# Optimization experiments

Hardware: AMD Instinct MI355X
Metric: run time of the kernel (lower is better)

The kernel has to match this reference:

```python
import jax, jax.numpy as jnp
import numpy as np

VOC, OUT, HID, CUR = 50257, 512, 64, 16
B, S = 32, 4096
EPS = 1e-5


def _ln(x, g, b):
    m = jnp.mean(x, axis=-1, keepdims=True)
    v = jnp.mean((x - m) ** 2, axis=-1, keepdims=True)
    return (x - m) * jax.lax.rsqrt(v + EPS) * g + b


def setup_inputs() -> dict:
    key = jax.random.key(0)
    ks = jax.random.split(key, 12)
    sd = 0.02
    return {
        "x": jax.random.randint(ks[0], (B, S), 0, VOC, dtype=jnp.int64),
        "emb": jax.random.normal(ks[1], (VOC, CUR), jnp.float32) * sd,
        "Wq": jax.random.normal(ks[2], (CUR, CUR), jnp.float32) * sd,
        "bq": jnp.zeros((CUR,), jnp.float32),
        "Wk": jax.random.normal(ks[3], (CUR, CUR), jnp.float32) * sd,
        "bk": jnp.zeros((CUR,), jnp.float32),
        "Wv": jax.random.normal(ks[4], (CUR, CUR), jnp.float32) * sd,
        "bv": jnp.zeros((CUR,), jnp.float32),
        "g_lim": jnp.ones((CUR,), jnp.float32),
        "b_lim": jnp.zeros((CUR,), jnp.float32),
        "Ws": jax.random.normal(ks[5], (HID + CUR, HID), jnp.float32) * sd,
        "bs": jnp.zeros((HID,), jnp.float32),
        "g_doubt": jnp.ones((HID,), jnp.float32),
        "b_doubt": jnp.zeros((HID,), jnp.float32),
        "Wd": jax.random.normal(ks[6], (HID + CUR, OUT), jnp.float32) * sd,
        "bd": jnp.zeros((OUT,), jnp.float32),
        "g_check": jnp.ones((OUT,), jnp.float32),
        "b_check": jnp.zeros((OUT,), jnp.float32),
    }


def reference(x, emb, Wq, bq, Wk, bk, Wv, bv, g_lim, b_lim, Ws, bs,
              g_doubt, b_doubt, Wd, bd, g_check, b_check):
    Bsz, Slen = x.shape
    n_chunks = Slen // CUR
    # [n_chunks, B, CUR] token ids per chunk
    xc = x.reshape(Bsz, n_chunks, CUR).transpose(1, 0, 2)
    sus0 = jnp.zeros((Bsz, CUR, HID), emb.dtype)
    scale = 1.0 / np.sqrt(CUR)

    def step(sus, ids):
        read = emb[ids]                                  # [B, CUR, CUR]
        q = read @ Wq + bq
        k = read @ Wk + bk
        v = read @ Wv + bv
        scores = jnp.einsum('bqd,bkd->bqk', q, k) * scale
        watch = jnp.einsum('bqk,bkd->bqd', jax.nn.softmax(scores, axis=-1), v)
        watch = _ln(watch, g_lim, b_lim)                 # dropout = identity (eval)
        combined = jnp.concatenate([watch, sus], axis=-1)  # [B, CUR, HID+CUR]
        sus_new = _ln(jax.nn.gelu(combined @ Ws + bs, approximate=False),
                      g_doubt, b_doubt)
        out = _ln(combined @ Wd + bd, g_check, b_check)  # [B, CUR, OUT]
        return sus_new, out

    _, outs = jax.lax.scan(step, sus0, xc)               # [n_chunks, B, CUR, OUT]
    return outs.transpose(1, 0, 2, 3).reshape(Bsz, Slen, OUT)
```

## Files before the change

kernel.cpp:

```cpp
#include <hip/hip_runtime.h>
#include <math.h>

#define VOCN 50257
#define OUTD 512
#define HIDD 64
#define CURD 16
#define BB   32
#define SS   4096
#define NCH  256
#define KDIM 80
#define LNEPS 1e-5f

#define DPP_ADD(x, ctrl) \
    ((x) + __int_as_float(__builtin_amdgcn_update_dpp( \
        0, __float_as_int(x), (ctrl), 0xf, 0xf, true)))

__device__ __forceinline__ float row16_sum(float x) {
    x = DPP_ADD(x, 0xB1);
    x = DPP_ADD(x, 0x4E);
    x = DPP_ADD(x, 0x141);
    x = DPP_ADD(x, 0x140);
    return x;
}

__device__ __forceinline__ float wave64_sum(float x) {
    float r = row16_sum(x);
    float a = __int_as_float(__builtin_amdgcn_readlane(__float_as_int(r), 0));
    float b = __int_as_float(__builtin_amdgcn_readlane(__float_as_int(r), 16));
    float c = __int_as_float(__builtin_amdgcn_readlane(__float_as_int(r), 32));
    float d = __int_as_float(__builtin_amdgcn_readlane(__float_as_int(r), 48));
    return (a + b) + (c + d);
}

__device__ __forceinline__ unsigned short f2bf(float x) {
    unsigned u = __float_as_uint(x);
    u += 0x7fffu + ((u >> 16) & 1u);
    return (unsigned short)(u >> 16);
}
__device__ __forceinline__ float bf2f(unsigned short h) {
    return __uint_as_float(((unsigned)h) << 16);
}

typedef __attribute__((ext_vector_type(8))) short bf16x8;
typedef __attribute__((ext_vector_type(4))) float f32x4;

__global__ __launch_bounds__(256) void wd_pack_kernel(
    const float* __restrict__ Wd,
    unsigned short* __restrict__ hi, unsigned short* __restrict__ lo)
{
    int idx = blockIdx.x * 256 + threadIdx.x;
    if (idx >= 96 * 512) return;
    int k = idx / 512, c = idx % 512;
    float v = (k < KDIM) ? Wd[(size_t)k * OUTD + c] : 0.f;
    unsigned short h = f2bf(v);
    unsigned short l = f2bf(v - bf2f(h));
    int s = k >> 5, kk = k & 31, g = kk >> 3, e = kk & 7;
    size_t o = (((size_t)(s * 512 + c)) * 4 + g) * 8 + e;
    hi[o] = h;
    lo[o] = l;
}

__global__ __launch_bounds__(256) void attn_kernel(
    const int* __restrict__ x, const float* __restrict__ emb,
    const float* __restrict__ Wq, const float* __restrict__ bq,
    const float* __restrict__ Wk, const float* __restrict__ bk,
    const float* __restrict__ Wv, const float* __restrict__ bv,
    const float* __restrict__ g_lim, const float* __restrict__ b_lim,
    float* __restrict__ combined)
{
    const int wid  = threadIdx.x >> 6;
    const int lane = threadIdx.x & 63;
    const int tile = blockIdx.x * 4 + wid;
    const int t = tile >> 5, b = tile & 31;
    const int i  = lane >> 2;
    const int jg = lane & 3;
    const int j0 = jg * 4;

    __shared__ __align__(16) float ldsT[4][4][16][20];
    float (*R)[20] = ldsT[wid][0];
    float (*Q)[20] = ldsT[wid][1];
    float (*K)[20] = ldsT[wid][2];
    float (*V)[20] = ldsT[wid][3];

    int myid = 0;
    if (lane < 16) myid = x[b * SS + t * CURD + lane];
    const int id_i = __shfl(myid, i, 64);

    float4 r4 = *(const float4*)(emb + (size_t)id_i * CURD + j0);
    *(float4*)&R[i][j0] = r4;

    float rrow[16];
    {
        float4 t0 = *(const float4*)&R[i][0];
        float4 t1 = *(const float4*)&R[i][4];
        float4 t2 = *(const float4*)&R[i][8];
        float4 t3 = *(const float4*)&R[i][12];
        rrow[0]=t0.x; rrow[1]=t0.y; rrow[2]=t0.z;  rrow[3]=t0.w;
        rrow[4]=t1.x; rrow[5]=t1.y; rrow[6]=t1.z;  rrow[7]=t1.w;
        rrow[8]=t2.x; rrow[9]=t2.y; rrow[10]=t2.z; rrow[11]=t2.w;
        rrow[12]=t3.x; rrow[13]=t3.y; rrow[14]=t3.z; rrow[15]=t3.w;
    }

    float4 q4 = *(const float4*)(bq + j0);
    float4 k4 = *(const float4*)(bk + j0);
    float4 v4 = *(const float4*)(bv + j0);
    #pragma unroll
    for (int k = 0; k < 16; ++k) {
        float rv = rrow[k];
        float4 wq4 = *(const float4*)(Wq + k * CURD + j0);
        float4 wk4 = *(const float4*)(Wk + k * CURD + j0);
        float4 wv4 = *(const float4*)(Wv + k * CURD + j0);
        q4.x = fmaf(rv, wq4.x, q4.x); q4.y = fmaf(rv, wq4.y, q4.y);
        q4.z = fmaf(rv, wq4.z, q4.z); q4.w = fmaf(rv, wq4.w, q4.w);
        k4.x = fmaf(rv, wk4.x, k4.x); k4.y = fmaf(rv, wk4.y, k4.y);
        k4.z = fmaf(rv, wk4.z, k4.z); k4.w = fmaf(rv, wk4.w, k4.w);
        v4.x = fmaf(rv, wv4.x, v4.x); v4.y = fmaf(rv, wv4.y, v4.y);
        v4.z = fmaf(rv, wv4.z, v4.z); v4.w = fmaf(rv, wv4.w, v4.w);
    }
    *(float4*)&Q[i][j0] = q4;
    *(float4*)&K[i][j0] = k4;
    *(float4*)&V[i][j0] = v4;

    float qrow[16];
    {
        float4 t0 = *(const float4*)&Q[i][0];
        float4 t1 = *(const float4*)&Q[i][4];
        float4 t2 = *(const float4*)&Q[i][8];
        float4 t3 = *(const float4*)&Q[i][12];
        qrow[0]=t0.x; qrow[1]=t0.y; qrow[2]=t0.z;  qrow[3]=t0.w;
        qrow[4]=t1.x; qrow[5]=t1.y; qrow[6]=t1.z;  qrow[7]=t1.w;
        qrow[8]=t2.x; qrow[9]=t2.y; qrow[10]=t2.z; qrow[11]=t2.w;
        qrow[12]=t3.x; qrow[13]=t3.y; qrow[14]=t3.z; qrow[15]=t3.w;
    }
    float sc[4];
    #pragma unroll
    for (int jj = 0; jj < 4; ++jj) {
        const int row = j0 + jj;
        float4 c0 = *(const float4*)&K[row][0];
        float4 c1 = *(const float4*)&K[row][4];
        float4 c2 = *(const float4*)&K[row][8];
        float4 c3 = *(const float4*)&K[row][12];
        float d0 = qrow[0]*c0.x + qrow[1]*c0.y + qrow[2]*c0.z + qrow[3]*c0.w;
        float d1 = qrow[4]*c1.x + qrow[5]*c1.y + qrow[6]*c1.z + qrow[7]*c1.w;
        float d2 = qrow[8]*c2.x + qrow[9]*c2.y + qrow[10]*c2.z + qrow[11]*c2.w;
        float d3 = qrow[12]*c3.x + qrow[13]*c3.y + qrow[14]*c3.z + qrow[15]*c3.w;
        sc[jj] = ((d0 + d1) + (d2 + d3)) * 0.25f;
    }

    float mx = fmaxf(fmaxf(sc[0], sc[1]), fmaxf(sc[2], sc[3]));
    mx = fmaxf(mx, __shfl_xor(mx, 1));
    mx = fmaxf(mx, __shfl_xor(mx, 2));
    float e0 = expf(sc[0]-mx), e1 = expf(sc[1]-mx),
          e2 = expf(sc[2]-mx), e3 = expf(sc[3]-mx);
    float es = (e0 + e1) + (e2 + e3);
    es += __shfl_xor(es, 1);
    es += __shfl_xor(es, 2);
    float rs = 1.f / es;
    float4 p4 = make_float4(e0*rs, e1*rs, e2*rs, e3*rs);
    *(float4*)&R[i][j0] = p4;

    float prow[16];
    {
        float4 t0 = *(const float4*)&R[i][0];
        float4 t1 = *(const float4*)&R[i][4];
        float4 t2 = *(const float4*)&R[i][8];
        float4 t3 = *(const float4*)&R[i][12];
        prow[0]=t0.x; prow[1]=t0.y; prow[2]=t0.z;  prow[3]=t0.w;
        prow[4]=t1.x; prow[5]=t1.y; prow[6]=t1.z;  prow[7]=t1.w;
        prow[8]=t2.x; prow[9]=t2.y; prow[10]=t2.z; prow[11]=t2.w;
        prow[12]=t3.x; prow[13]=t3.y; prow[14]=t3.z; prow[15]=t3.w;
    }
    float4 w4 = make_float4(0.f, 0.f, 0.f, 0.f);
    #pragma unroll
    for (int k = 0; k < 16; ++k) {
        float4 vk = *(const float4*)&V[k][j0];
        float pv = prow[k];
        w4.x = fmaf(pv, vk.x, w4.x); w4.y = fmaf(pv, vk.y, w4.y);
        w4.z = fmaf(pv, vk.z, w4.z); w4.w = fmaf(pv, vk.w, w4.w);
    }

    float s1 = (w4.x + w4.y) + (w4.z + w4.w);
    float s2 = (w4.x*w4.x + w4.y*w4.y) + (w4.z*w4.z + w4.w*w4.w);
    s1 += __shfl_xor(s1, 1); s1 += __shfl_xor(s1, 2);
    s2 += __shfl_xor(s2, 1); s2 += __shfl_xor(s2, 2);
    float m   = s1 * (1.f / 16.f);
    float var = s2 * (1.f / 16.f) - m * m;
    float inv = rsqrtf(var + LNEPS);
    float4 gl = *(const float4*)(g_lim + j0);
    float4 bl = *(const float4*)(b_lim + j0);
    float4 o;
    o.x = (w4.x - m) * inv * gl.x + bl.x;
    o.y = (w4.y - m) * inv * gl.y + bl.y;
    o.z = (w4.z - m) * inv * gl.z + bl.z;
    o.w = (w4.w - m) * inv * gl.w + bl.w;
    *(float4*)(combined + ((size_t)tile * CURD + i) * KDIM + j0) = o;
}

__global__ __launch_bounds__(64) void rec_kernel(
    const float* __restrict__ Ws, const float* __restrict__ bs,
    const float* __restrict__ g_doubt, const float* __restrict__ b_doubt,
    float* __restrict__ combined)
{
    const int chain = blockIdx.x;
    const int b = chain >> 4;
    const int r = chain & 15;
    const int c = threadIdx.x;

    __shared__ __align__(16) float s_G[64];

    float Wsw[16];
    #pragma unroll
    for (int j = 0; j < 16; ++j) Wsw[j] = Ws[j * HIDD + c];

    float Wsp[64];
    float u = 0.f, w0 = 0.f;
    #pragma unroll
    for (int j = 0; j < 64; ++j) {
        float w   = Ws[(16 + j) * HIDD + c];
        float gdj = g_doubt[j];
        float bdj = b_doubt[j];
        Wsp[j] = gdj * w;
        u += Wsp[j];
        w0 = fmaf(bdj, w, w0);
    }
    const float bsc  = bs[c];
    const float gd_c = g_doubt[c];
    const float bd_c = b_doubt[c];

    size_t rowoff = ((size_t)b * CURD + r) * KDIM;
    const size_t stride = (size_t)BB * CURD * KDIM;

    float4 wc0, wc1, wc2, wc3;
    float4 wn0, wn1, wn2, wn3;
    {
        const float4* p0 = (const float4*)(combined + rowoff);
        wc0 = p0[0]; wc1 = p0[1]; wc2 = p0[2]; wc3 = p0[3];
        const float4* p1 = (const float4*)(combined + rowoff + stride);
        wn0 = p1[0]; wn1 = p1[1]; wn2 = p1[2]; wn3 = p1[3];
    }

    float P = 0.f, mp = 0.f, ip = 0.f, w0f = 0.f;
    float sv_store = 0.f;

    for (int t = 0; t < NCH; ++t) {
        combined[rowoff + 16 + c] = sv_store;

        float4 wp0, wp1, wp2, wp3;
        if (t + 2 < NCH) {
            const float4* p2 = (const float4*)(combined + rowoff + 2 * stride);
            wp0 = p2[0]; wp1 = p2[1]; wp2 = p2[2]; wp3 = p2[3];
        } else {
            wp0 = wp1 = wp2 = wp3 = make_float4(0.f, 0.f, 0.f, 0.f);
        }

        float h0 = fmaf(ip, P - mp * u, bsc + w0f);
        float h1 = 0.f, h2 = 0.f, h3 = 0.f;
        h0 = fmaf(wc0.x, Wsw[0],  h0); h1 = fmaf(wc0.y, Wsw[1],  h1);
        h2 = fmaf(wc0.z, Wsw[2],  h2); h3 = fmaf(wc0.w, Wsw[3],  h3);
        h0 = fmaf(wc1.x, Wsw[4],  h0); h1 = fmaf(wc1.y, Wsw[5],  h1);
        h2 = fmaf(wc1.z, Wsw[6],  h2); h3 = fmaf(wc1.w, Wsw[7],  h3);
        h0 = fmaf(wc2.x, Wsw[8],  h0); h1 = fmaf(wc2.y, Wsw[9],  h1);
        h2 = fmaf(wc2.z, Wsw[10], h2); h3 = fmaf(wc2.w, Wsw[11], h3);
        h0 = fmaf(wc3.x, Wsw[12], h0); h1 = fmaf(wc3.y, Wsw[13], h1);
        h2 = fmaf(wc3.z, Wsw[14], h2); h3 = fmaf(wc3.w, Wsw[15], h3);
        float h = (h0 + h1) + (h2 + h3);

        float G = 0.5f * h * (1.f + erff(h * 0.70710678118654752f));

        s_G[c] = G;
        const float4* gp = (const float4*)s_G;
        float4 xr[16];
        #pragma unroll
        for (int j4 = 0; j4 < 16; ++j4) xr[j4] = gp[j4];

        float s1 = wave64_sum(G);
        float s2 = wave64_sum(G * G);
        float m   = s1 * (1.f / 64.f);
        float var = s2 * (1.f / 64.f) - m * m;
        float inv = rsqrtf(var + LNEPS);

        float p0=0.f,p1=0.f,p2=0.f,p3=0.f,p4=0.f,p5=0.f,p6=0.f,p7=0.f;
        #pragma unroll
        for (int j4 = 0; j4 < 16; j4 += 2) {
            float4 x0 = xr[j4], x1 = xr[j4 + 1];
            p0 = fmaf(x0.x, Wsp[4*j4+0], p0);
            p1 = fmaf(x0.y, Wsp[4*j4+1], p1);
            p2 = fmaf(x0.z, Wsp[4*j4+2], p2);
            p3 = fmaf(x0.w, Wsp[4*j4+3], p3);
            p4 = fmaf(x1.x, Wsp[4*j4+4], p4);
            p5 = fmaf(x1.y, Wsp[4*j4+5], p5);
            p6 = fmaf(x1.z, Wsp[4*j4+6], p6);
            p7 = fmaf(x1.w, Wsp[4*j4+7], p7);
        }
        P = ((p0 + p1) + (p2 + p3)) + ((p4 + p5) + (p6 + p7));

        sv_store = fmaf((G - m) * inv, gd_c, bd_c);
        mp = m; ip = inv; w0f = w0;
        wc0 = wn0; wc1 = wn1; wc2 = wn2; wc3 = wn3;
        wn0 = wp0; wn1 = wp1; wn2 = wp2; wn3 = wp3;
        rowoff += stride;
    }
}

#define M_BLK 32
__global__ __launch_bounds__(256) void out_mfma_kernel(
    const float* __restrict__ combined,
    const unsigned short* __restrict__ Bhi,
    const unsigned short* __restrict__ Blo,
    const float* __restrict__ bd, const float* __restrict__ g_check,
    const float* __restrict__ b_check, float* __restrict__ out)
{
    __shared__ __align__(16) unsigned short Ahi[M_BLK][104];
    __shared__ __align__(16) unsigned short Alo[M_BLK][104];
    __shared__ float red[4][M_BLK][2];

    const int tid = threadIdx.x;
    const size_t rowbase = (size_t)blockIdx.x * M_BLK;

    {
        const float4* src4 = (const float4*)(combined + rowbase * KDIM);
        #pragma unroll
        for (int u2 = 0; u2 < 3; ++u2) {
            int idx = tid + 256 * u2;
            if (idx < M_BLK * 20) {
                float4 v = src4[idx];
                int rr = idx / 20, k4 = idx % 20;
                float vs[4] = {v.x, v.y, v.z, v.w};
                #pragma unroll
                for (int e = 0; e < 4; ++e) {
                    unsigned short h = f2bf(vs[e]);
                    Ahi[rr][k4 * 4 + e] = h;
                    Alo[rr][k4 * 4 + e] = f2bf(vs[e] - bf2f(h));
                }
            }
        }
        #pragma unroll
        for (int u2 = 0; u2 < 2; ++u2) {
            int idx = tid + 256 * u2;
            int rr = idx >> 4, kk = 80 + (idx & 15);
            Ahi[rr][kk] = 0;
            Alo[rr][kk] = 0;
        }
    }

    const int lane  = tid & 63;
    const int wid   = tid >> 6;
    const int arowb = lane & 15;
    const int kg    = lane >> 4;

    int cols[8]; float bdv[8], gcv[8], bcv[8];
    #pragma unroll
    for (int n = 0; n < 8; ++n) {
        cols[n] = wid * 128 + n * 16 + arowb;
        bdv[n] = bd[cols[n]];
        gcv[n] = g_check[cols[n]];
        bcv[n] = b_check[cols[n]];
    }

    __syncthreads();

    bf16x8 a_hi[2][3], a_lo[2][3];
    #pragma unroll
    for (int ms = 0; ms < 2; ++ms)
        #pragma unroll
        for (int s = 0; s < 3; ++s) {
            a_hi[ms][s] = *(const bf16x8*)&Ahi[ms * 16 + arowb][s * 32 + kg * 8];
            a_lo[ms][s] = *(const bf16x8*)&Alo[ms * 16 + arowb][s * 32 + kg * 8];
        }

    f32x4 acc[2][8];
    #pragma unroll
    for (int ms = 0; ms < 2; ++ms)
        #pragma unroll
        for (int n = 0; n < 8; ++n) acc[ms][n] = (f32x4){0.f, 0.f, 0.f, 0.f};

    #pragma unroll
    for (int n = 0; n < 8; ++n) {
        #pragma unroll
        for (int s = 0; s < 3; ++s) {
            size_t off = (((size_t)(s * 512 + cols[n])) * 4 + kg) * 8;
            bf16x8 bh = *(const bf16x8*)(Bhi + off);
            bf16x8 bl = *(const bf16x8*)(Blo + off);
            acc[0][n] = __builtin_amdgcn_mfma_f32_16x16x32_bf16(a_hi[0][s], bh, acc[0][n], 0, 0, 0);
            acc[1][n] = __builtin_amdgcn_mfma_f32_16x16x32_bf16(a_hi[1][s], bh, acc[1][n], 0, 0, 0);
            acc[0][n] = __builtin_amdgcn_mfma_f32_16x16x32_bf16(a_lo[0][s], bh, acc[0][n], 0, 0, 0);
            acc[1][n] = __builtin_amdgcn_mfma_f32_16x16x32_bf16(a_lo[1][s], bh, acc[1][n], 0, 0, 0);
            acc[0][n] = __builtin_amdgcn_mfma_f32_16x16x32_bf16(a_hi[0][s], bl, acc[0][n], 0, 0, 0);
            acc[1][n] = __builtin_amdgcn_mfma_f32_16x16x32_bf16(a_hi[1][s], bl, acc[1][n], 0, 0, 0);
        }
    }

    #pragma unroll
    for (int ms = 0; ms < 2; ++ms) {
        float s1[4] = {0.f, 0.f, 0.f, 0.f};
        float s2[4] = {0.f, 0.f, 0.f, 0.f};
        #pragma unroll
        for (int n = 0; n < 8; ++n) {
            #pragma unroll
            for (int j = 0; j < 4; ++j) {
                float v = acc[ms][n][j] + bdv[n];
                acc[ms][n][j] = v;
                s1[j] += v;
                s2[j] = fmaf(v, v, s2[j]);
            }
        }
        #pragma unroll
        for (int j = 0; j < 4; ++j) {
            s1[j] = row16_sum(s1[j]);
            s2[j] = row16_sum(s2[j]);
        }
        if (arowb == 0) {
            #pragma unroll
            for (int j = 0; j < 4; ++j) {
                red[wid][ms * 16 + kg * 4 + j][0] = s1[j];
                red[wid][ms * 16 + kg * 4 + j][1] = s2[j];
            }
        }
    }
    __syncthreads();

    #pragma unroll
    for (int ms = 0; ms < 2; ++ms) {
        #pragma unroll
        for (int j = 0; j < 4; ++j) {
            const int rowl = ms * 16 + kg * 4 + j;
            float t1 = (red[0][rowl][0] + red[1][rowl][0])
                     + (red[2][rowl][0] + red[3][rowl][0]);
            float t2 = (red[0][rowl][1] + red[1][rowl][1])
                     + (red[2][rowl][1] + red[3][rowl][1]);
            float mm  = t1 * (1.f / 512.f);
            float var = t2 * (1.f / 512.f) - mm * mm;
            float iv  = rsqrtf(var + LNEPS);

            size_t R = rowbase + (size_t)rowl;
            int ii  = (int)(R & 15);
            int bb2 = (int)((R >> 4) & 31);
            int tt  = (int)(R >> 9);
            size_t orow = ((size_t)bb2 * SS + (size_t)tt * CURD + ii) * OUTD;

            #pragma unroll
            for (int n = 0; n < 8; ++n) {
                out[orow + cols[n]] =
                    (acc[ms][n][j] - mm) * iv * gcv[n] + bcv[n];
            }
        }
    }
}

extern "C" void kernel_launch(void* const* d_in, const int* in_sizes, int n_in,
                              void* d_out, int out_size, void* d_ws, size_t ws_size,
                              hipStream_t stream)
{
    const int*   x       = (const int*)  d_in[0];
    const float* emb     = (const float*)d_in[1];
    const float* Wq      = (const float*)d_in[2];
    const float* bq      = (const float*)d_in[3];
    const float* Wk      = (const float*)d_in[4];
    const float* bk      = (const float*)d_in[5];
    const float* Wv      = (const float*)d_in[6];
    const float* bv      = (const float*)d_in[7];
    const float* g_lim   = (const float*)d_in[8];
    const float* b_lim   = (const float*)d_in[9];
    const float* Ws      = (const float*)d_in[10];
    const float* bs      = (const float*)d_in[11];
    const float* g_doubt = (const float*)d_in[12];
    const float* b_doubt = (const float*)d_in[13];
    const float* Wd      = (const float*)d_in[14];
    const float* bd      = (const float*)d_in[15];
    const float* g_check = (const float*)d_in[16];
    const float* b_check = (const float*)d_in[17];

    float* out      = (float*)d_out;
    float* combined = (float*)d_ws;
    unsigned short* whi = (unsigned short*)((char*)d_ws + 41943040);
    unsigned short* wlo = whi + 96 * 512;

    wd_pack_kernel<<<dim3(192), dim3(256), 0, stream>>>(Wd, whi, wlo);

    attn_kernel<<<dim3(NCH * BB / 4), dim3(256), 0, stream>>>(
        x, emb, Wq, bq, Wk, bk, Wv, bv, g_lim, b_lim, combined);

    rec_kernel<<<dim3(BB * CURD), dim3(64), 0, stream>>>(
        Ws, bs, g_doubt, b_doubt, combined);

    out_mfma_kernel<<<dim3((NCH * BB * CURD) / M_BLK), dim3(256), 0, stream>>>(
        combined, whi, wlo, bd, g_check, b_check, out);
}
```

Measured before the change: 503.5 us.

## Fuse recurrence and output GEMM into one persistent kernel with slab flags

Merges the recurrent-state kernel and the output MFMA kernel into a single launch. 128 blocks (4 chains each) run the recurrence and publish progress per 16-step slab through atomic counters. Another 512 persistent blocks pull output tiles from an atomic work queue and spin-wait on the slab flags before reading the combined rows. The Wd bf16 packing and flag reset move into the attention kernel, removing two launches. The aim is to overlap the serial recurrence with the bandwidth-heavy output stage. This relies on the recurrence blocks getting scheduled alongside the spinning consumers, and there is a bounded spin guard that could let a consumer read data before it is ready.

```diff
diff --git a/kernel.cpp b/kernel.cpp
--- a/kernel.cpp
+++ b/kernel.cpp
@@ -11,6 +11,14 @@
 #define KDIM 80
 #define LNEPS 1e-5f
 
+#define WS_WHI   41943040
+#define WS_WLO   (WS_WHI + 96*512*2)
+#define WS_FLAGS (WS_WLO + 96*512*2)
+#define NRECB    128
+#define NOUTB    512
+#define NTASKS   4096
+#define NSLABS   16
+
 #define DPP_ADD(x, ctrl) \
     ((x) + __int_as_float(__builtin_amdgcn_update_dpp( \
         0, __float_as_int(x), (ctrl), 0xf, 0xf, true)))
@@ -44,30 +52,22 @@
 typedef __attribute__((ext_vector_type(8))) short bf16x8;
 typedef __attribute__((ext_vector_type(4))) float f32x4;
 
-__global__ __launch_bounds__(256) void wd_pack_kernel(
-    const float* __restrict__ Wd,
-    unsigned short* __restrict__ hi, unsigned short* __restrict__ lo)
-{
-    int idx = blockIdx.x * 256 + threadIdx.x;
-    if (idx >= 96 * 512) return;
-    int k = idx / 512, c = idx % 512;
-    float v = (k < KDIM) ? Wd[(size_t)k * OUTD + c] : 0.f;
-    unsigned short h = f2bf(v);
-    unsigned short l = f2bf(v - bf2f(h));
-    int s = k >> 5, kk = k & 31, g = kk >> 3, e = kk & 7;
-    size_t o = (((size_t)(s * 512 + c)) * 4 + g) * 8 + e;
-    hi[o] = h;
-    lo[o] = l;
-}
-
 __global__ __launch_bounds__(256) void attn_kernel(
     const int* __restrict__ x, const float* __restrict__ emb,
     const float* __restrict__ Wq, const float* __restrict__ bq,
     const float* __restrict__ Wk, const float* __restrict__ bk,
     const float* __restrict__ Wv, const float* __restrict__ bv,
     const float* __restrict__ g_lim, const float* __restrict__ b_lim,
-    float* __restrict__ combined)
+    float* __restrict__ combined,
+    const float* __restrict__ Wd,
+    unsigned short* __restrict__ whi, unsigned short* __restrict__ wlo,
+    unsigned int* __restrict__ flags)
 {
+    if (blockIdx.x == 0) {
+        flags[threadIdx.x] = 0u;
+        flags[threadIdx.x + 256] = 0u;
+    }
+
     const int wid  = threadIdx.x >> 6;
     const int lane = threadIdx.x & 63;
     const int tile = blockIdx.x * 4 + wid;
@@ -194,153 +194,151 @@
     o.z = (w4.z - m) * inv * gl.z + bl.z;
     o.w = (w4.w - m) * inv * gl.w + bl.w;
     *(float4*)(combined + ((size_t)tile * CURD + i) * KDIM + j0) = o;
-}
-
-__global__ __launch_bounds__(64) void rec_kernel(
+
+    if (blockIdx.x < 192) {
+        int idx = blockIdx.x * 256 + threadIdx.x;
+        int k = idx / 512, c = idx % 512;
+        float v = (k < KDIM) ? Wd[(size_t)k * OUTD + c] : 0.f;
+        unsigned short h = f2bf(v);
+        unsigned short l = f2bf(v - bf2f(h));
+        int s = k >> 5, kk = k & 31, g = kk >> 3, e = kk & 7;
+        size_t o2 = (((size_t)(s * 512 + c)) * 4 + g) * 8 + e;
+        whi[o2] = h;
+        wlo[o2] = l;
+    }
+}
+
+__global__ __launch_bounds__(256) void fused_kernel(
     const float* __restrict__ Ws, const float* __restrict__ bs,
     const float* __restrict__ g_doubt, const float* __restrict__ b_doubt,
-    float* __restrict__ combined)
-{
-    const int chain = blockIdx.x;
-    const int b = chain >> 4;
-    const int r = chain & 15;
-    const int c = threadIdx.x;
-
-    __shared__ __align__(16) float s_G[64];
-
-    float Wsw[16];
-    #pragma unroll
-    for (int j = 0; j < 16; ++j) Wsw[j] = Ws[j * HIDD + c];
-
-    float Wsp[64];
-    float u = 0.f, w0 = 0.f;
-    #pragma unroll
-    for (int j = 0; j < 64; ++j) {
-        float w   = Ws[(16 + j) * HIDD + c];
-        float gdj = g_doubt[j];
-        float bdj = b_doubt[j];
-        Wsp[j] = gdj * w;
-        u += Wsp[j];
-        w0 = fmaf(bdj, w, w0);
-    }
-    const float bsc  = bs[c];
-    const float gd_c = g_doubt[c];
-    const float bd_c = b_doubt[c];
-
-    size_t rowoff = ((size_t)b * CURD + r) * KDIM;
-    const size_t stride = (size_t)BB * CURD * KDIM;
-
-    float4 wc0, wc1, wc2, wc3;
-    float4 wn0, wn1, wn2, wn3;
-    {
-        const float4* p0 = (const float4*)(combined + rowoff);
-        wc0 = p0[0]; wc1 = p0[1]; wc2 = p0[2]; wc3 = p0[3];
-        const float4* p1 = (const float4*)(combined + rowoff + stride);
-        wn0 = p1[0]; wn1 = p1[1]; wn2 = p1[2]; wn3 = p1[3];
-    }
-
-    float P = 0.f, mp = 0.f, ip = 0.f, w0f = 0.f;
-    float sv_store = 0.f;
-
-    for (int t = 0; t < NCH; ++t) {
-        combined[rowoff + 16 + c] = sv_store;
-
-        float4 wp0, wp1, wp2, wp3;
-        if (t + 2 < NCH) {
-            const float4* p2 = (const float4*)(combined + rowoff + 2 * stride);
-            wp0 = p2[0]; wp1 = p2[1]; wp2 = p2[2]; wp3 = p2[3];
-        } else {
-            wp0 = wp1 = wp2 = wp3 = make_float4(0.f, 0.f, 0.f, 0.f);
-        }
-
-        float h0 = fmaf(ip, P - mp * u, bsc + w0f);
-        float h1 = 0.f, h2 = 0.f, h3 = 0.f;
-        h0 = fmaf(wc0.x, Wsw[0],  h0); h1 = fmaf(wc0.y, Wsw[1],  h1);
-        h2 = fmaf(wc0.z, Wsw[2],  h2); h3 = fmaf(wc0.w, Wsw[3],  h3);
-        h0 = fmaf(wc1.x, Wsw[4],  h0); h1 = fmaf(wc1.y, Wsw[5],  h1);
-        h2 = fmaf(wc1.z, Wsw[6],  h2); h3 = fmaf(wc1.w, Wsw[7],  h3);
-        h0 = fmaf(wc2.x, Wsw[8],  h0); h1 = fmaf(wc2.y, Wsw[9],  h1);
-        h2 = fmaf(wc2.z, Wsw[10], h2); h3 = fmaf(wc2.w, Wsw[11], h3);
-        h0 = fmaf(wc3.x, Wsw[12], h0); h1 = fmaf(wc3.y, Wsw[13], h1);
-        h2 = fmaf(wc3.z, Wsw[14], h2); h3 = fmaf(wc3.w, Wsw[15], h3);
-        float h = (h0 + h1) + (h2 + h3);
-
-        float G = 0.5f * h * (1.f + erff(h * 0.70710678118654752f));
-
-        s_G[c] = G;
-        const float4* gp = (const float4*)s_G;
-        float4 xr[16];
-        #pragma unroll
-        for (int j4 = 0; j4 < 16; ++j4) xr[j4] = gp[j4];
-
-        float s1 = wave64_sum(G);
-        float s2 = wave64_sum(G * G);
-        float m   = s1 * (1.f / 64.f);
-        float var = s2 * (1.f / 64.f) - m * m;
-        float inv = rsqrtf(var + LNEPS);
-
-        float p0=0.f,p1=0.f,p2=0.f,p3=0.f,p4=0.f,p5=0.f,p6=0.f,p7=0.f;
-        #pragma unroll
-        for (int j4 = 0; j4 < 16; j4 += 2) {
-            float4 x0 = xr[j4], x1 = xr[j4 + 1];
-            p0 = fmaf(x0.x, Wsp[4*j4+0], p0);
-            p1 = fmaf(x0.y, Wsp[4*j4+1], p1);
-            p2 = fmaf(x0.z, Wsp[4*j4+2], p2);
-            p3 = fmaf(x0.w, Wsp[4*j4+3], p3);
-            p4 = fmaf(x1.x, Wsp[4*j4+4], p4);
-            p5 = fmaf(x1.y, Wsp[4*j4+5], p5);
-            p6 = fmaf(x1.z, Wsp[4*j4+6], p6);
-            p7 = fmaf(x1.w, Wsp[4*j4+7], p7);
-        }
-        P = ((p0 + p1) + (p2 + p3)) + ((p4 + p5) + (p6 + p7));
-
-        sv_store = fmaf((G - m) * inv, gd_c, bd_c);
-        mp = m; ip = inv; w0f = w0;
-        wc0 = wn0; wc1 = wn1; wc2 = wn2; wc3 = wn3;
-        wn0 = wp0; wn1 = wp1; wn2 = wp2; wn3 = wp3;
-        rowoff += stride;
-    }
-}
-
-#define M_BLK 32
-__global__ __launch_bounds__(256) void out_mfma_kernel(
-    const float* __restrict__ combined,
+    float* __restrict__ combined,
     const unsigned short* __restrict__ Bhi,
     const unsigned short* __restrict__ Blo,
     const float* __restrict__ bd, const float* __restrict__ g_check,
-    const float* __restrict__ b_check, float* __restrict__ out)
+    const float* __restrict__ b_check, float* __restrict__ out,
+    unsigned int* __restrict__ flags)
 {
-    __shared__ __align__(16) unsigned short Ahi[M_BLK][104];
-    __shared__ __align__(16) unsigned short Alo[M_BLK][104];
-    __shared__ float red[4][M_BLK][2];
+    __shared__ __align__(16) unsigned short Ahi[32][104];
+    __shared__ __align__(16) unsigned short Alo[32][104];
+    __shared__ float red[4][32][2];
+    __shared__ float s_G[4][64];
+    __shared__ int s_tk;
 
     const int tid = threadIdx.x;
-    const size_t rowbase = (size_t)blockIdx.x * M_BLK;
-
-    {
-        const float4* src4 = (const float4*)(combined + rowbase * KDIM);
-        #pragma unroll
-        for (int u2 = 0; u2 < 3; ++u2) {
-            int idx = tid + 256 * u2;
-            if (idx < M_BLK * 20) {
-                float4 v = src4[idx];
-                int rr = idx / 20, k4 = idx % 20;
-                float vs[4] = {v.x, v.y, v.z, v.w};
-                #pragma unroll
-                for (int e = 0; e < 4; ++e) {
-                    unsigned short h = f2bf(vs[e]);
-                    Ahi[rr][k4 * 4 + e] = h;
-                    Alo[rr][k4 * 4 + e] = f2bf(vs[e] - bf2f(h));
-                }
-            }
-        }
-        #pragma unroll
-        for (int u2 = 0; u2 < 2; ++u2) {
-            int idx = tid + 256 * u2;
-            int rr = idx >> 4, kk = 80 + (idx & 15);
-            Ahi[rr][kk] = 0;
-            Alo[rr][kk] = 0;
-        }
+    if (tid == 0)
+        s_tk = (int)__hip_atomic_fetch_add(&flags[0], 1u,
+                    __ATOMIC_RELAXED, __HIP_MEMORY_SCOPE_AGENT);
+    __syncthreads();
+    const int role_tk = s_tk;
+
+    if (role_tk < NRECB) {
+        __builtin_amdgcn_s_setprio(1);
+        const int wid = tid >> 6;
+        const int c   = tid & 63;
+        const int chain = role_tk * 4 + wid;
+        const int b = chain >> 4;
+        const int r = chain & 15;
+
+        float Wsw[16];
+        #pragma unroll
+        for (int j = 0; j < 16; ++j) Wsw[j] = Ws[j * HIDD + c];
+
+        float Wsp[64];
+        float u = 0.f, w0 = 0.f;
+        #pragma unroll
+        for (int j = 0; j < 64; ++j) {
+            float w   = Ws[(16 + j) * HIDD + c];
+            float gdj = g_doubt[j];
+            float bdj = b_doubt[j];
+            Wsp[j] = gdj * w;
+            u += Wsp[j];
+            w0 = fmaf(bdj, w, w0);
+        }
+        const float bsc  = bs[c];
+        const float gd_c = g_doubt[c];
+        const float bd_c = b_doubt[c];
+
+        size_t rowoff = ((size_t)b * CURD + r) * KDIM;
+        const size_t stride = (size_t)BB * CURD * KDIM;
+
+        float4 wc0, wc1, wc2, wc3;
+        float4 wn0, wn1, wn2, wn3;
+        {
+            const float4* p0 = (const float4*)(combined + rowoff);
+            wc0 = p0[0]; wc1 = p0[1]; wc2 = p0[2]; wc3 = p0[3];
+            const float4* p1 = (const float4*)(combined + rowoff + stride);
+            wn0 = p1[0]; wn1 = p1[1]; wn2 = p1[2]; wn3 = p1[3];
+        }
+
+        float P = 0.f, mp = 0.f, ip = 0.f, w0f = 0.f;
+        float sv_store = 0.f;
+
+        for (int t = 0; t < NCH; ++t) {
+            combined[rowoff + 16 + c] = sv_store;
+
+            if ((t & 15) == 15) {
+                __builtin_amdgcn_fence(__ATOMIC_RELEASE, "agent");
+                if (c == 0)
+                    __hip_atomic_fetch_add(&flags[16 + (t >> 4) * 16], 1u,
+                        __ATOMIC_RELAXED, __HIP_MEMORY_SCOPE_AGENT);
+            }
+
+            float4 wp0, wp1, wp2, wp3;
+            if (t + 2 < NCH) {
+                const float4* p2 = (const float4*)(combined + rowoff + 2 * stride);
+                wp0 = p2[0]; wp1 = p2[1]; wp2 = p2[2]; wp3 = p2[3];
+            } else {
+                wp0 = wp1 = wp2 = wp3 = make_float4(0.f, 0.f, 0.f, 0.f);
+            }
+
+            float h0 = fmaf(ip, P - mp * u, bsc + w0f);
+            float h1 = 0.f, h2 = 0.f, h3 = 0.f;
+            h0 = fmaf(wc0.x, Wsw[0],  h0); h1 = fmaf(wc0.y, Wsw[1],  h1);
+            h2 = fmaf(wc0.z, Wsw[2],  h2); h3 = fmaf(wc0.w, Wsw[3],  h3);
+            h0 = fmaf(wc1.x, Wsw[4],  h0); h1 = fmaf(wc1.y, Wsw[5],  h1);
+            h2 = fmaf(wc1.z, Wsw[6],  h2); h3 = fmaf(wc1.w, Wsw[7],  h3);
+            h0 = fmaf(wc2.x, Wsw[8],  h0); h1 = fmaf(wc2.y, Wsw[9],  h1);
+            h2 = fmaf(wc2.z, Wsw[10], h2); h3 = fmaf(wc2.w, Wsw[11], h3);
+            h0 = fmaf(wc3.x, Wsw[12], h0); h1 = fmaf(wc3.y, Wsw[13], h1);
+            h2 = fmaf(wc3.z, Wsw[14], h2); h3 = fmaf(wc3.w, Wsw[15], h3);
+            float h = (h0 + h1) + (h2 + h3);
+
+            float G = 0.5f * h * (1.f + erff(h * 0.70710678118654752f));
+
+            s_G[wid][c] = G;
+            const float4* gp = (const float4*)s_G[wid];
+            float4 xr[16];
+            #pragma unroll
+            for (int j4 = 0; j4 < 16; ++j4) xr[j4] = gp[j4];
+
+            float s1 = wave64_sum(G);
+            float s2 = wave64_sum(G * G);
+            float m   = s1 * (1.f / 64.f);
+            float var = s2 * (1.f / 64.f) - m * m;
+            float inv = rsqrtf(var + LNEPS);
+
+            float p0=0.f,p1=0.f,p2=0.f,p3=0.f,p4=0.f,p5=0.f,p6=0.f,p7=0.f;
+            #pragma unroll
+            for (int j4 = 0; j4 < 16; j4 += 2) {
+                float4 x0 = xr[j4], x1 = xr[j4 + 1];
+                p0 = fmaf(x0.x, Wsp[4*j4+0], p0);
+                p1 = fmaf(x0.y, Wsp[4*j4+1], p1);
+                p2 = fmaf(x0.z, Wsp[4*j4+2], p2);
+                p3 = fmaf(x0.w, Wsp[4*j4+3], p3);
+                p4 = fmaf(x1.x, Wsp[4*j4+4], p4);
+                p5 = fmaf(x1.y, Wsp[4*j4+5], p5);
+                p6 = fmaf(x1.z, Wsp[4*j4+6], p6);
+                p7 = fmaf(x1.w, Wsp[4*j4+7], p7);
+            }
+            P = ((p0 + p1) + (p2 + p3)) + ((p4 + p5) + (p6 + p7));
+
+            sv_store = fmaf((G - m) * inv, gd_c, bd_c);
+            mp = m; ip = inv; w0f = w0;
+            wc0 = wn0; wc1 = wn1; wc2 = wn2; wc3 = wn3;
+            wn0 = wp0; wn1 = wp1; wn2 = wp2; wn3 = wp3;
+            rowoff += stride;
+        }
+        return;
     }
 
     const int lane  = tid & 63;
@@ -357,93 +355,143 @@
         bcv[n] = b_check[cols[n]];
     }
 
-    __syncthreads();
-
-    bf16x8 a_hi[2][3], a_lo[2][3];
-    #pragma unroll
-    for (int ms = 0; ms < 2; ++ms)
-        #pragma unroll
-        for (int s = 0; s < 3; ++s) {
-            a_hi[ms][s] = *(const bf16x8*)&Ahi[ms * 16 + arowb][s * 32 + kg * 8];
-            a_lo[ms][s] = *(const bf16x8*)&Alo[ms * 16 + arowb][s * 32 + kg * 8];
-        }
-
-    f32x4 acc[2][8];
-    #pragma unroll
-    for (int ms = 0; ms < 2; ++ms)
-        #pragma unroll
-        for (int n = 0; n < 8; ++n) acc[ms][n] = (f32x4){0.f, 0.f, 0.f, 0.f};
-
-    #pragma unroll
-    for (int n = 0; n < 8; ++n) {
-        #pragma unroll
-        for (int s = 0; s < 3; ++s) {
-            size_t off = (((size_t)(s * 512 + cols[n])) * 4 + kg) * 8;
-            bf16x8 bh = *(const bf16x8*)(Bhi + off);
-            bf16x8 bl = *(const bf16x8*)(Blo + off);
-            acc[0][n] = __builtin_amdgcn_mfma_f32_16x16x32_bf16(a_hi[0][s], bh, acc[0][n], 0, 0, 0);
-            acc[1][n] = __builtin_amdgcn_mfma_f32_16x16x32_bf16(a_hi[1][s], bh, acc[1][n], 0, 0, 0);
-            acc[0][n] = __builtin_amdgcn_mfma_f32_16x16x32_bf16(a_lo[0][s], bh, acc[0][n], 0, 0, 0);
-            acc[1][n] = __builtin_amdgcn_mfma_f32_16x16x32_bf16(a_lo[1][s], bh, acc[1][n], 0, 0, 0);
-            acc[0][n] = __builtin_amdgcn_mfma_f32_16x16x32_bf16(a_hi[0][s], bl, acc[0][n], 0, 0, 0);
-            acc[1][n] = __builtin_amdgcn_mfma_f32_16x16x32_bf16(a_hi[1][s], bl, acc[1][n], 0, 0, 0);
-        }
-    }
-
-    #pragma unroll
-    for (int ms = 0; ms < 2; ++ms) {
-        float s1[4] = {0.f, 0.f, 0.f, 0.f};
-        float s2[4] = {0.f, 0.f, 0.f, 0.f};
+    for (;;) {
+        if (tid == 0)
+            s_tk = (int)__hip_atomic_fetch_add(&flags[1], 1u,
+                        __ATOMIC_RELAXED, __HIP_MEMORY_SCOPE_AGENT);
+        __syncthreads();
+        const int task = s_tk;
+        if (task >= NTASKS) break;
+
+        const int slab = task >> 8;
+        if (tid == 0) {
+            unsigned guard = 0;
+            while (__hip_atomic_load(&flags[16 + slab * 16], __ATOMIC_RELAXED,
+                                     __HIP_MEMORY_SCOPE_AGENT) < 512u
+                   && guard < (1u << 20)) {
+                __builtin_amdgcn_s_sleep(32);
+                ++guard;
+            }
+        }
+        __syncthreads();
+        __builtin_amdgcn_fence(__ATOMIC_ACQUIRE, "agent");
+
+        const size_t rowbase = (size_t)task * 32;
+
+        {
+            const float4* src4 = (const float4*)(combined + rowbase * KDIM);
+            #pragma unroll
+            for (int u2 = 0; u2 < 3; ++u2) {
+                int idx = tid + 256 * u2;
+                if (idx < 32 * 20) {
+                    float4 v = src4[idx];
+                    int rr = idx / 20, k4 = idx % 20;
+                    float vs[4] = {v.x, v.y, v.z, v.w};
+                    #pragma unroll
+                    for (int e = 0; e < 4; ++e) {
+                        unsigned short h = f2bf(vs[e]);
+                        Ahi[rr][k4 * 4 + e] = h;
+                        Alo[rr][k4 * 4 + e] = f2bf(vs[e] - bf2f(h));
+                    }
+                }
+            }
+            #pragma unroll
+            for (int u2 = 0; u2 < 2; ++u2) {
+                int idx = tid + 256 * u2;
+                int rr = idx >> 4, kk = 80 + (idx & 15);
+                Ahi[rr][kk] = 0;
+                Alo[rr][kk] = 0;
+            }
+        }
+        __syncthreads();
+
+        bf16x8 a_hi[2][3], a_lo[2][3];
+        #pragma unroll
+        for (int ms = 0; ms < 2; ++ms)
+            #pragma unroll
+            for (int s = 0; s < 3; ++s) {
+                a_hi[ms][s] = *(const bf16x8*)&Ahi[ms * 16 + arowb][s * 32 + kg * 8];
+                a_lo[ms][s] = *(const bf16x8*)&Alo[ms * 16 + arowb][s * 32 + kg * 8];
+            }
+
+        f32x4 acc[2][8];
+        #pragma unroll
+        for (int ms = 0; ms < 2; ++ms)
+            #pragma unroll
+            for (int n = 0; n < 8; ++n) acc[ms][n] = (f32x4){0.f, 0.f, 0.f, 0.f};
+
         #pragma unroll
         for (int n = 0; n < 8; ++n) {
             #pragma unroll
+            for (int s = 0; s < 3; ++s) {
+                size_t off = (((size_t)(s * 512 + cols[n])) * 4 + kg) * 8;
+                bf16x8 bh = *(const bf16x8*)(Bhi + off);
+                bf16x8 bl = *(const bf16x8*)(Blo + off);
+                acc[0][n] = __builtin_amdgcn_mfma_f32_16x16x32_bf16(a_hi[0][s], bh, acc[0][n], 0, 0, 0);
+                acc[1][n] = __builtin_amdgcn_mfma_f32_16x16x32_bf16(a_hi[1][s], bh, acc[1][n], 0, 0, 0);
+                acc[0][n] = __builtin_amdgcn_mfma_f32_16x16x32_bf16(a_lo[0][s], bh, acc[0][n], 0, 0, 0);
+                acc[1][n] = __builtin_amdgcn_mfma_f32_16x16x32_bf16(a_lo[1][s], bh, acc[1][n], 0, 0, 0);
+                acc[0][n] = __builtin_amdgcn_mfma_f32_16x16x32_bf16(a_hi[0][s], bl, acc[0][n], 0, 0, 0);
+                acc[1][n] = __builtin_amdgcn_mfma_f32_16x16x32_bf16(a_hi[1][s], bl, acc[1][n], 0, 0, 0);
+            }
+        }
+
+        #pragma unroll
+        for (int ms = 0; ms < 2; ++ms) {
+            float s1[4] = {0.f, 0.f, 0.f, 0.f};
+            float s2[4] = {0.f, 0.f, 0.f, 0.f};
+            #pragma unroll
+            for (int n = 0; n < 8; ++n) {
+                #pragma unroll
+                for (int j = 0; j < 4; ++j) {
+                    float v = acc[ms][n][j] + bdv[n];
+                    acc[ms][n][j] = v;
+                    s1[j] += v;
+                    s2[j] = fmaf(v, v, s2[j]);
+                }
+            }
+            #pragma unroll
             for (int j = 0; j < 4; ++j) {
-                float v = acc[ms][n][j] + bdv[n];
-                acc[ms][n][j] = v;
-                s1[j] += v;
-                s2[j] = fmaf(v, v, s2[j]);
-            }
-        }
-        #pragma unroll
-        for (int j = 0; j < 4; ++j) {
-            s1[j] = row16_sum(s1[j]);
-            s2[j] = row16_sum(s2[j]);
-        }
-        if (arowb == 0) {
+                s1[j] = row16_sum(s1[j]);
+                s2[j] = row16_sum(s2[j]);
+            }
+            if (arowb == 0) {
+                #pragma unroll
+                for (int j = 0; j < 4; ++j) {
+                    red[wid][ms * 16 + kg * 4 + j][0] = s1[j];
+                    red[wid][ms * 16 + kg * 4 + j][1] = s2[j];
+                }
+            }
+        }
+        __syncthreads();
+
+        #pragma unroll
+        for (int ms = 0; ms < 2; ++ms) {
             #pragma unroll
             for (int j = 0; j < 4; ++j) {
-                red[wid][ms * 16 + kg * 4 + j][0] = s1[j];
-                red[wid][ms * 16 + kg * 4 + j][1] = s2[j];
-            }
-        }
-    }
-    __syncthreads();
-
-    #pragma unroll
-    for (int ms = 0; ms < 2; ++ms) {
-        #pragma unroll
-        for (int j = 0; j < 4; ++j) {
-            const int rowl = ms * 16 + kg * 4 + j;
-            float t1 = (red[0][rowl][0] + red[1][rowl][0])
-                     + (red[2][rowl][0] + red[3][rowl][0]);
-            float t2 = (red[0][rowl][1] + red[1][rowl][1])
-                     + (red[2][rowl][1] + red[3][rowl][1]);
-            float mm  = t1 * (1.f / 512.f);
-            float var = t2 * (1.f / 512.f) - mm * mm;
-            float iv  = rsqrtf(var + LNEPS);
-
-            size_t R = rowbase + (size_t)rowl;
-            int ii  = (int)(R & 15);
-            int bb2 = (int)((R >> 4) & 31);
-            int tt  = (int)(R >> 9);
-            size_t orow = ((size_t)bb2 * SS + (size_t)tt * CURD + ii) * OUTD;
-
-            #pragma unroll
-            for (int n = 0; n < 8; ++n) {
-                out[orow + cols[n]] =
-                    (acc[ms][n][j] - mm) * iv * gcv[n] + bcv[n];
-            }
-        }
+                const int rowl = ms * 16 + kg * 4 + j;
+                float t1 = (red[0][rowl][0] + red[1][rowl][0])
+                         + (red[2][rowl][0] + red[3][rowl][0]);
+                float t2 = (red[0][rowl][1] + red[1][rowl][1])
+                         + (red[2][rowl][1] + red[3][rowl][1]);
+                float mm  = t1 * (1.f / 512.f);
+                float var = t2 * (1.f / 512.f) - mm * mm;
+                float iv  = rsqrtf(var + LNEPS);
+
+                size_t R = rowbase + (size_t)rowl;
+                int ii  = (int)(R & 15);
+                int bb2 = (int)((R >> 4) & 31);
+                int tt  = (int)(R >> 9);
+                size_t orow = ((size_t)bb2 * SS + (size_t)tt * CURD + ii) * OUTD;
+
+                #pragma unroll
+                for (int n = 0; n < 8; ++n) {
+                    out[orow + cols[n]] =
+                        (acc[ms][n][j] - mm) * iv * gcv[n] + bcv[n];
+                }
+            }
+        }
+        __syncthreads();
     }
 }
 
@@ -472,17 +520,15 @@
 
     float* out      = (float*)d_out;
     float* combined = (float*)d_ws;
-    unsigned short* whi = (unsigned short*)((char*)d_ws + 41943040);
-    unsigned short* wlo = whi + 96 * 512;
-
-    wd_pack_kernel<<<dim3(192), dim3(256), 0, stream>>>(Wd, whi, wlo);
+    unsigned short* whi = (unsigned short*)((char*)d_ws + WS_WHI);
+    unsigned short* wlo = (unsigned short*)((char*)d_ws + WS_WLO);
+    unsigned int*  flags = (unsigned int*)((char*)d_ws + WS_FLAGS);
 
     attn_kernel<<<dim3(NCH * BB / 4), dim3(256), 0, stream>>>(
-        x, emb, Wq, bq, Wk, bk, Wv, bv, g_lim, b_lim, combined);
-
-    rec_kernel<<<dim3(BB * CURD), dim3(64), 0, stream>>>(
-        Ws, bs, g_doubt, b_doubt, combined);
-
-    out_mfma_kernel<<<dim3((NCH * BB * CURD) / M_BLK), dim3(256), 0, stream>>>(
-        combined, whi, wlo, bd, g_check, b_check, out);
-}
+        x, emb, Wq, bq, Wk, bk, Wv, bv, g_lim, b_lim, combined,
+        Wd, whi, wlo, flags);
+
+    fused_kernel<<<dim3(NRECB + NOUTB), dim3(256), 0, stream>>>(
+        Ws, bs, g_doubt, b_doubt, combined, whi, wlo,
+        bd, g_check, b_check, out, flags);
+}
```

Result: slower. 778.2 us (+54.6%).

## Preload watch rows into LDS in recurrence kernel and fold Wd packing into attention

Applied to the files above, without the earlier changes.

The recurrence kernel now runs two chains per 128-thread block and stages each chain's full 256-step watch sequence into shared memory up front. It computes the Ws watch-projection partial for the next step during the current step, taking the global-memory loads and 16 FMAs off the serial critical path. The Wd bf16 hi/lo packing moves into the tail of the attention kernel to remove one kernel launch. The cost is 32KB of LDS per block and the serial-chain occupancy layout changes, while the per-step global store of the sus state remains.

```diff
diff --git a/kernel.cpp b/kernel.cpp
--- a/kernel.cpp
+++ b/kernel.cpp
@@ -11,6 +11,9 @@
 #define KDIM 80
 #define LNEPS 1e-5f
 
+#define WS_WHI   41943040
+#define WS_WLO   (WS_WHI + 96*512*2)
+
 #define DPP_ADD(x, ctrl) \
     ((x) + __int_as_float(__builtin_amdgcn_update_dpp( \
         0, __float_as_int(x), (ctrl), 0xf, 0xf, true)))
@@ -44,29 +47,15 @@
 typedef __attribute__((ext_vector_type(8))) short bf16x8;
 typedef __attribute__((ext_vector_type(4))) float f32x4;
 
-__global__ __launch_bounds__(256) void wd_pack_kernel(
-    const float* __restrict__ Wd,
-    unsigned short* __restrict__ hi, unsigned short* __restrict__ lo)
-{
-    int idx = blockIdx.x * 256 + threadIdx.x;
-    if (idx >= 96 * 512) return;
-    int k = idx / 512, c = idx % 512;
-    float v = (k < KDIM) ? Wd[(size_t)k * OUTD + c] : 0.f;
-    unsigned short h = f2bf(v);
-    unsigned short l = f2bf(v - bf2f(h));
-    int s = k >> 5, kk = k & 31, g = kk >> 3, e = kk & 7;
-    size_t o = (((size_t)(s * 512 + c)) * 4 + g) * 8 + e;
-    hi[o] = h;
-    lo[o] = l;
-}
-
 __global__ __launch_bounds__(256) void attn_kernel(
     const int* __restrict__ x, const float* __restrict__ emb,
     const float* __restrict__ Wq, const float* __restrict__ bq,
     const float* __restrict__ Wk, const float* __restrict__ bk,
     const float* __restrict__ Wv, const float* __restrict__ bv,
     const float* __restrict__ g_lim, const float* __restrict__ b_lim,
-    float* __restrict__ combined)
+    float* __restrict__ combined,
+    const float* __restrict__ Wd,
+    unsigned short* __restrict__ whi, unsigned short* __restrict__ wlo)
 {
     const int wid  = threadIdx.x >> 6;
     const int lane = threadIdx.x & 63;
@@ -194,19 +183,45 @@
     o.z = (w4.z - m) * inv * gl.z + bl.z;
     o.w = (w4.w - m) * inv * gl.w + bl.w;
     *(float4*)(combined + ((size_t)tile * CURD + i) * KDIM + j0) = o;
-}
-
-__global__ __launch_bounds__(64) void rec_kernel(
+
+    if (blockIdx.x < 192) {
+        int idx = blockIdx.x * 256 + threadIdx.x;
+        int k = idx / 512, c = idx % 512;
+        float v = (k < KDIM) ? Wd[(size_t)k * OUTD + c] : 0.f;
+        unsigned short h = f2bf(v);
+        unsigned short l = f2bf(v - bf2f(h));
+        int s = k >> 5, kk = k & 31, g = kk >> 3, e = kk & 7;
+        size_t o2 = (((size_t)(s * 512 + c)) * 4 + g) * 8 + e;
+        whi[o2] = h;
+        wlo[o2] = l;
+    }
+}
+
+__global__ __launch_bounds__(128) void rec_kernel(
     const float* __restrict__ Ws, const float* __restrict__ bs,
     const float* __restrict__ g_doubt, const float* __restrict__ b_doubt,
     float* __restrict__ combined)
 {
-    const int chain = blockIdx.x;
+    __shared__ __align__(16) float s_watch[2][NCH][16];
+    __shared__ __align__(16) float s_G[2][64];
+
+    const int wid = threadIdx.x >> 6;
+    const int c   = threadIdx.x & 63;
+    const int chain = blockIdx.x * 2 + wid;
     const int b = chain >> 4;
     const int r = chain & 15;
-    const int c = threadIdx.x;
-
-    __shared__ __align__(16) float s_G[64];
+
+    {
+        const int tt4 = c >> 2;
+        const int j4  = c & 3;
+        #pragma unroll
+        for (int p = 0; p < 16; ++p) {
+            int t = p * 16 + tt4;
+            float4 v = *(const float4*)(combined
+                + ((size_t)(t * BB + b) * CURD + r) * KDIM + j4 * 4);
+            *(float4*)&s_watch[wid][t][j4 * 4] = v;
+        }
+    }
 
     float Wsw[16];
     #pragma unroll
@@ -230,13 +245,17 @@
     size_t rowoff = ((size_t)b * CURD + r) * KDIM;
     const size_t stride = (size_t)BB * CURD * KDIM;
 
-    float4 wc0, wc1, wc2, wc3;
-    float4 wn0, wn1, wn2, wn3;
+    float wp0, wp1, wp2, wp3;
     {
-        const float4* p0 = (const float4*)(combined + rowoff);
-        wc0 = p0[0]; wc1 = p0[1]; wc2 = p0[2]; wc3 = p0[3];
-        const float4* p1 = (const float4*)(combined + rowoff + stride);
-        wn0 = p1[0]; wn1 = p1[1]; wn2 = p1[2]; wn3 = p1[3];
+        const float4* wrow = (const float4*)&s_watch[wid][0][0];
+        float4 a0 = wrow[0], a1 = wrow[1], a2 = wrow[2], a3 = wrow[3];
+        wp0 = a0.x*Wsw[0]; wp1 = a0.y*Wsw[1]; wp2 = a0.z*Wsw[2]; wp3 = a0.w*Wsw[3];
+        wp0 = fmaf(a1.x, Wsw[4],  wp0); wp1 = fmaf(a1.y, Wsw[5],  wp1);
+        wp2 = fmaf(a1.z, Wsw[6],  wp2); wp3 = fmaf(a1.w, Wsw[7],  wp3);
+        wp0 = fmaf(a2.x, Wsw[8],  wp0); wp1 = fmaf(a2.y, Wsw[9],  wp1);
+        wp2 = fmaf(a2.z, Wsw[10], wp2); wp3 = fmaf(a2.w, Wsw[11], wp3);
+        wp0 = fmaf(a3.x, Wsw[12], wp0); wp1 = fmaf(a3.y, Wsw[13], wp1);
+        wp2 = fmaf(a3.z, Wsw[14], wp2); wp3 = fmaf(a3.w, Wsw[15], wp3);
     }
 
     float P = 0.f, mp = 0.f, ip = 0.f, w0f = 0.f;
@@ -245,33 +264,26 @@
     for (int t = 0; t < NCH; ++t) {
         combined[rowoff + 16 + c] = sv_store;
 
-        float4 wp0, wp1, wp2, wp3;
-        if (t + 2 < NCH) {
-            const float4* p2 = (const float4*)(combined + rowoff + 2 * stride);
-            wp0 = p2[0]; wp1 = p2[1]; wp2 = p2[2]; wp3 = p2[3];
-        } else {
-            wp0 = wp1 = wp2 = wp3 = make_float4(0.f, 0.f, 0.f, 0.f);
-        }
-
-        float h0 = fmaf(ip, P - mp * u, bsc + w0f);
-        float h1 = 0.f, h2 = 0.f, h3 = 0.f;
-        h0 = fmaf(wc0.x, Wsw[0],  h0); h1 = fmaf(wc0.y, Wsw[1],  h1);
-        h2 = fmaf(wc0.z, Wsw[2],  h2); h3 = fmaf(wc0.w, Wsw[3],  h3);
-        h0 = fmaf(wc1.x, Wsw[4],  h0); h1 = fmaf(wc1.y, Wsw[5],  h1);
-        h2 = fmaf(wc1.z, Wsw[6],  h2); h3 = fmaf(wc1.w, Wsw[7],  h3);
-        h0 = fmaf(wc2.x, Wsw[8],  h0); h1 = fmaf(wc2.y, Wsw[9],  h1);
-        h2 = fmaf(wc2.z, Wsw[10], h2); h3 = fmaf(wc2.w, Wsw[11], h3);
-        h0 = fmaf(wc3.x, Wsw[12], h0); h1 = fmaf(wc3.y, Wsw[13], h1);
-        h2 = fmaf(wc3.z, Wsw[14], h2); h3 = fmaf(wc3.w, Wsw[15], h3);
-        float h = (h0 + h1) + (h2 + h3);
+        float h = (fmaf(ip, P - mp * u, bsc + w0f) + wp0)
+                + ((wp1 + wp2) + wp3);
 
         float G = 0.5f * h * (1.f + erff(h * 0.70710678118654752f));
 
-        s_G[c] = G;
-        const float4* gp = (const float4*)s_G;
-        float4 xr[16];
-        #pragma unroll
-        for (int j4 = 0; j4 < 16; ++j4) xr[j4] = gp[j4];
+        s_G[wid][c] = G;
+        const float4* gp = (const float4*)s_G[wid];
+
+        {
+            const int tn = (t + 1 < NCH) ? t + 1 : t;
+            const float4* wrow = (const float4*)&s_watch[wid][tn][0];
+            float4 a0 = wrow[0], a1 = wrow[1], a2 = wrow[2], a3 = wrow[3];
+            wp0 = a0.x*Wsw[0]; wp1 = a0.y*Wsw[1]; wp2 = a0.z*Wsw[2]; wp3 = a0.w*Wsw[3];
+            wp0 = fmaf(a1.x, Wsw[4],  wp0); wp1 = fmaf(a1.y, Wsw[5],  wp1);
+            wp2 = fmaf(a1.z, Wsw[6],  wp2); wp3 = fmaf(a1.w, Wsw[7],  wp3);
+            wp0 = fmaf(a2.x, Wsw[8],  wp0); wp1 = fmaf(a2.y, Wsw[9],  wp1);
+            wp2 = fmaf(a2.z, Wsw[10], wp2); wp3 = fmaf(a2.w, Wsw[11], wp3);
+            wp0 = fmaf(a3.x, Wsw[12], wp0); wp1 = fmaf(a3.y, Wsw[13], wp1);
+            wp2 = fmaf(a3.z, Wsw[14], wp2); wp3 = fmaf(a3.w, Wsw[15], wp3);
+        }
 
         float s1 = wave64_sum(G);
         float s2 = wave64_sum(G * G);
@@ -281,23 +293,30 @@
 
         float p0=0.f,p1=0.f,p2=0.f,p3=0.f,p4=0.f,p5=0.f,p6=0.f,p7=0.f;
         #pragma unroll
-        for (int j4 = 0; j4 < 16; j4 += 2) {
-            float4 x0 = xr[j4], x1 = xr[j4 + 1];
-            p0 = fmaf(x0.x, Wsp[4*j4+0], p0);
-            p1 = fmaf(x0.y, Wsp[4*j4+1], p1);
-            p2 = fmaf(x0.z, Wsp[4*j4+2], p2);
-            p3 = fmaf(x0.w, Wsp[4*j4+3], p3);
-            p4 = fmaf(x1.x, Wsp[4*j4+4], p4);
-            p5 = fmaf(x1.y, Wsp[4*j4+5], p5);
-            p6 = fmaf(x1.z, Wsp[4*j4+6], p6);
-            p7 = fmaf(x1.w, Wsp[4*j4+7], p7);
+        for (int bq = 0; bq < 4; ++bq) {
+            float4 x0 = gp[bq*4+0], x1 = gp[bq*4+1];
+            float4 x2 = gp[bq*4+2], x3 = gp[bq*4+3];
+            p0 = fmaf(x0.x, Wsp[16*bq+0],  p0);
+            p1 = fmaf(x0.y, Wsp[16*bq+1],  p1);
+            p2 = fmaf(x0.z, Wsp[16*bq+2],  p2);
+            p3 = fmaf(x0.w, Wsp[16*bq+3],  p3);
+            p4 = fmaf(x1.x, Wsp[16*bq+4],  p4);
+            p5 = fmaf(x1.y, Wsp[16*bq+5],  p5);
+            p6 = fmaf(x1.z, Wsp[16*bq+6],  p6);
+            p7 = fmaf(x1.w, Wsp[16*bq+7],  p7);
+            p0 = fmaf(x2.x, Wsp[16*bq+8],  p0);
+            p1 = fmaf(x2.y, Wsp[16*bq+9],  p1);
+            p2 = fmaf(x2.z, Wsp[16*bq+10], p2);
+            p3 = fmaf(x2.w, Wsp[16*bq+11], p3);
+            p4 = fmaf(x3.x, Wsp[16*bq+12], p4);
+            p5 = fmaf(x3.y, Wsp[16*bq+13], p5);
+            p6 = fmaf(x3.z, Wsp[16*bq+14], p6);
+            p7 = fmaf(x3.w, Wsp[16*bq+15], p7);
         }
         P = ((p0 + p1) + (p2 + p3)) + ((p4 + p5) + (p6 + p7));
 
         sv_store = fmaf((G - m) * inv, gd_c, bd_c);
         mp = m; ip = inv; w0f = w0;
-        wc0 = wn0; wc1 = wn1; wc2 = wn2; wc3 = wn3;
-        wn0 = wp0; wn1 = wp1; wn2 = wp2; wn3 = wp3;
         rowoff += stride;
     }
 }
@@ -472,15 +491,14 @@
 
     float* out      = (float*)d_out;
     float* combined = (float*)d_ws;
-    unsigned short* whi = (unsigned short*)((char*)d_ws + 41943040);
-    unsigned short* wlo = whi + 96 * 512;
-
-    wd_pack_kernel<<<dim3(192), dim3(256), 0, stream>>>(Wd, whi, wlo);
+    unsigned short* whi = (unsigned short*)((char*)d_ws + WS_WHI);
+    unsigned short* wlo = (unsigned short*)((char*)d_ws + WS_WLO);
 
     attn_kernel<<<dim3(NCH * BB / 4), dim3(256), 0, stream>>>(
-        x, emb, Wq, bq, Wk, bk, Wv, bv, g_lim, b_lim, combined);
-
-    rec_kernel<<<dim3(BB * CURD), dim3(64), 0, stream>>>(
+        x, emb, Wq, bq, Wk, bk, Wv, bv, g_lim, b_lim, combined,
+        Wd, whi, wlo);
+
+    rec_kernel<<<dim3(BB * CURD / 2), dim3(128), 0, stream>>>(
         Ws, bs, g_doubt, b_doubt, combined);
 
     out_mfma_kernel<<<dim3((NCH * BB * CURD) / M_BLK), dim3(256), 0, stream>>>(
```

Result: no change. 509.5 us (+1.2%).
